# Kernel optimization log

Hardware: AMD Instinct MI355X
Metric: run time of the kernel (lower is better)

Reference implementation:

```python
import jax, jax.numpy as jnp
import numpy as np
from jax import lax

RES = 512          # resolution
L = 16             # n_light
M = 4
N = 2 * M          # Fourier series terms
FOCAL = 50.0
CAMD = 2.7         # camera_distance
WINDOW = 1.0
SHADOW_THR = 0.008
RES_OPT = 256      # resolution_optimize
OFFSET = -0.0642233295781
CLAMP = 0.4458709375254
RBLUR = 10         # gaussian blur radius (static)

FOV = 2.0 * np.arctan(0.5 * 36.0 / FOCAL)
TANH = np.tan(FOV / 2.0)
NEAR = CAMD - np.sqrt(2.0) * CAMD * TANH
FAR = CAMD + np.sqrt(2.0) * CAMD * TANH

_rot_pi = np.array([[np.cos(np.pi), 0, np.sin(np.pi), 0], [0, 1, 0, 0],
                    [-np.sin(np.pi), 0, np.cos(np.pi), 0], [0, 0, 0, 1]], np.float32)
_m_dist = np.eye(4, dtype=np.float32); _m_dist[2, 3] = -CAMD
_local = (_rot_pi @ _m_dist).astype(np.float32)
_orth = np.array([[1.0 / WINDOW, 0, 0, 0], [0, 1.0 / WINDOW, 0, 0],
                  [0, 0, -2.0 / (FAR - NEAR), -(FAR + NEAR) / (FAR - NEAR)],
                  [0, 0, 0, 1]], np.float32)
_ck = (np.pi * (2.0 * (np.arange(M) + 1) - 1)).astype(np.float32)  # [M]


def _rotate_xyz_light(dirs):
    # dirs: [L,3] -> [L,4,4] (already transposed as in the torch permute(0,2,1))
    xd, yd, zd = dirs[:, 0], dirs[:, 1], dirs[:, 2]
    cosp = jnp.sqrt(xd * xd + zd * zd)
    cost = zd / cosp
    sint = xd / cosp
    Z = jnp.zeros_like(xd); O = jnp.ones_like(xd)
    Rn = jnp.stack([cost, -sint * yd, cosp * sint, Z,
                    Z, cosp, yd, Z,
                    -sint, -cost * yd, cosp * cost, Z,
                    Z, Z, Z, O], axis=-1).reshape(-1, 4, 4)
    return jnp.swapaxes(Rn, 1, 2)


def _blur_one(img, k):
    # img: [N,H,W], k: [2R+1]  separable gaussian, zero padding
    kh = k.reshape(1, 1, -1, 1)
    kw = k.reshape(1, 1, 1, -1)
    x = img[:, None]  # [N,1,H,W]
    x = lax.conv_general_dilated(x, kh, (1, 1), ((RBLUR, RBLUR), (0, 0)))
    x = lax.conv_general_dilated(x, kw, (1, 1), ((0, 0), (RBLUR, RBLUR)))
    return x[:, 0]


def _forward(depth, als, mask, z_map):
    res = RES
    local = jnp.asarray(_local); m_dist = jnp.asarray(_m_dist); orth = jnp.asarray(_orth)
    m1 = 2.0 * (jnp.arange(res, dtype=jnp.float32) / res + 1.0 / (2 * res)) - 1.0
    dz = depth[0, 0]                               # [res,res]
    px = -dz * TANH * m1[None, :]                  # x varies along width
    py = dz * TANH * m1[:, None]                   # y varies along height
    posw = jnp.stack([px, py, dz, jnp.ones_like(dz)], axis=-1).reshape(-1, 4)  # [V,4]
    posw_c = posw @ local.T

    mv = jnp.einsum('xy,dyz->dxz', m_dist, _rotate_xyz_light(als[:, :3]))  # [L,4,4]
    pfl = jnp.einsum('vw,dxw->dvx', posw_c, mv)
    pfl = jnp.einsum('dvw,xw->dvx', pfl, orth)      # [L,V,4]

    u = jnp.clip((res * (pfl[..., 0] + 1.0) * 0.5).astype(jnp.int32), 0, res - 1)
    v = jnp.clip((res * (pfl[..., 1] + 1.0) * 0.5).astype(jnp.int32), 0, res - 1)
    d = jnp.clip(0.5 * (1.0 + pfl[..., 2] / pfl[..., 3]), 0.0, 1.0)  # [L,V]

    li = jnp.arange(L)
    zg = z_map[li[:, None], v, u]                   # gather shadow-map depth [L,V]
    f = jnp.where(jnp.clip(d - zg, 0.0, None) > SHADOW_THR, 0.0, 1.0)

    ck = jnp.asarray(_ck)[None, :, None]            # [1,M,1]
    a_even = -2.0 * jnp.sin(ck * (d[:, None, :] + OFFSET)) / ck
    a_odd = 2.0 * jnp.cos(ck * (d[:, None, :] + OFFSET)) / ck
    a = jnp.stack([a_even, a_odd], axis=2).reshape(L, N, -1)  # interleaved [L,N,V]

    ckz = ck[..., None] * z_map[:, None]            # [L,M,res,res]
    B = jnp.stack([jnp.cos(ckz), jnp.sin(ckz)], axis=2).reshape(L, N, res, res)

    sig = (res / RES_OPT * (6.0 * als[:, 3] + 1.0) - 1.0) / 6.0   # [L]
    t = jnp.arange(-RBLUR, RBLUR + 1, dtype=jnp.float32)
    kern = jnp.exp(-0.5 * (t[None, :] / sig[:, None]) ** 2)
    kern = kern / jnp.sum(kern, axis=1, keepdims=True)            # [L,2R+1]
    D_map = jax.vmap(_blur_one)(B, kern)            # [L,N,res,res]

    ni = jnp.arange(N)
    D = D_map[li[:, None, None], ni[None, :, None], v[:, None, :], u[:, None, :]]  # [L,N,V]
    q = jnp.clip(jnp.sum(a * D, axis=1), -CLAMP, CLAMP) / CLAMP
    sf = 0.5 * (q + 1.0)

    hard = f.reshape(1, L, res, res)
    soft = jnp.clip(sf, 0.0, 1.0).reshape(1, L, res, res)
    return mask * hard, mask * soft


def setup_inputs() -> dict:
    key = jax.random.key(0)
    k1, k2, k3, k4, k5, k6 = jax.random.split(key, 6)
    depth = 2.0 + jax.random.uniform(k1, (1, 1, RES, RES), dtype=jnp.float32)
    mask = (jax.random.uniform(k2, (1, 1, RES, RES)) > 0.2).astype(jnp.float32)
    dirs = jax.random.normal(k3, (L, 3), dtype=jnp.float32)
    dirs = dirs / jnp.linalg.norm(dirs, axis=1, keepdims=True)
    sigma = 0.02 + 0.1 * jax.random.uniform(k4, (L, 1), dtype=jnp.float32)
    intensity = jax.random.uniform(k5, (L, 3), dtype=jnp.float32)
    als = jnp.concatenate([dirs, sigma, intensity], axis=1)  # [L,7]
    z_map = 0.3 + 0.7 * jax.random.uniform(k6, (L, RES, RES), dtype=jnp.float32)
    return {"depth": depth, "als": als, "mask": mask, "z_map": z_map}


def reference(depth, als, mask, z_map):
    return _forward(depth, als, mask, z_map)
```

## Files before the change

### kernel.cpp

```cpp
#include <hip/hip_runtime.h>
#include <math.h>


#define RESN 512
#define NL 16
#define NPIX (RESN*RESN)

__global__ void setup_kernel(const float* __restrict__ als,
                             float* __restrict__ lp) {
  #pragma clang fp contract(off)
  int l = (int)threadIdx.x;
  if (l >= NL) return;
  float xd = als[l*7+0], yd = als[l*7+1], zd = als[l*7+2], sg = als[l*7+3];
  float cosp = sqrtf(xd*xd + zd*zd);
  float cost = zd / cosp;
  float sint = xd / cosp;
  float* o = lp + l*16;
  o[0] = cost;
  o[1] = -sint;
  o[2] = (-sint)*yd;
  o[3] = cosp;
  o[4] = (-cost)*yd;
  o[5] = cosp*sint;
  o[6] = yd;
  o[7] = cosp*cost;
  float sig = ((2.0f*(6.0f*sg + 1.0f)) - 1.0f) / 6.0f;
  float ivs = 1.0f/(sig*sig);
  float e1  = __builtin_amdgcn_exp2f(-0.72134752044448170368f*ivs);
  float e1sq = e1*e1;
  float e2  = e1sq*e1sq;
  float kinv = 1.0f/(1.0f + 2.0f*e1 + 2.0f*e2);
  float w1n = e1*kinv;
  o[8] = kinv;
  o[9] = w1n;
  o[10] = (w1n >= 0.0056f) ? 1.0f : 0.0f;
  o[11] = kinv*kinv;
  o[12] = o[13] = o[14] = o[15] = 0.0f;
}

__global__ __launch_bounds__(128) void fused_kernel(
    const float* __restrict__ depth,
    const float* __restrict__ mask,
    const float* __restrict__ z_map,
    const float* __restrict__ lp,
    float* __restrict__ out,
    float TANHF, float OZF, float OWF)
{
  #pragma clang fp contract(off)
  const float OFFS = -0.0642233295781f;
  const float CLB  = 0.4458709375254f;
  const float TWO_OVER_PI = 0.63661977236758134308f;
  const int id = (int)blockIdx.x;
  const int l0 = id & 7;
  const int p  = ((id >> 3) << 7) + (int)threadIdx.x;
  const int r  = p >> 9, c = p & 511;

  float dz = depth[p];
  float mk = mask[p];
  float m1c = 2.0f * ((float)c / 512.0f + 0.0009765625f) - 1.0f;
  float m1r = 2.0f * ((float)r / 512.0f + 0.0009765625f) - 1.0f;
  float tT = dz * TANHF;
  float qx = tT * m1c;
  float qy = tT * m1r;
  float qz = 2.7f - dz;
  const bool live = (mk != 0.0f);

  #pragma unroll
  for (int k = 0; k < 2; ++k) {
    const int l = l0 + (k << 3);
    const int base = l << 18;
    float hard_out = 0.0f, soft_out = 0.0f;
    if (live) {
      const float* P = lp + l*16;
      float e00 = P[0], e02 = P[1], e10 = P[2], e11 = P[3], e12 = P[4];
      float e20 = P[5], e21 = P[6], e22 = P[7];
      float w0 = P[8], w1 = P[9];
      bool five_tap = P[10] != 0.0f;
      float w0sq = P[11];

      float X1 = fmaf(qz, e02, qx * e00);
      float Y1 = fmaf(qz, e12, fmaf(qy, e11, qx * e10));
      float T2 = fmaf(qz, e22, fmaf(qy, e21, qx * e20));
      float Z1 = T2 + (-2.7f);
      float ZZ = (Z1 * OZF) + OWF;
      float uf = (X1 + 1.0f) * 256.0f;
      float vf = (Y1 + 1.0f) * 256.0f;
      int u = (int)uf; u = u < 0 ? 0 : (u > 511 ? 511 : u);
      int v = (int)vf; v = v < 0 ? 0 : (v > 511 ? 511 : v);
      float dd = 0.5f * (1.0f + ZZ);
      dd = fminf(fmaxf(dd, 0.0f), 1.0f);
      float dpo = dd + OFFS;

      const float* zrC = z_map + base + (v << 9);
      float zg = zrC[u];

      auto fval = [&](float z) {
        float s = __builtin_amdgcn_sinf(0.5f * (z - dpo));
        float t = s * s;
        return s * fmaf(t, fmaf(t, fmaf(t, -9.142857142857142f, 19.2f),
                                -13.333333333333334f), 4.0f);
      };

      float q;
      if (five_tap) {
        int u0 = u > 0 ? u - 1 : 0;
        int u2 = u < 511 ? u + 1 : 511;
        int v0 = v > 0 ? v - 1 : 0;
        int v2 = v < 511 ? v + 1 : 511;
        float zT = z_map[base + (v0 << 9) + u];
        float zL = zrC[u0];
        float zR = zrC[u2];
        float zB = z_map[base + (v2 << 9) + u];
        float wuL = (u > 0)   ? w1 : 0.0f;
        float wuR = (u < 511) ? w1 : 0.0f;
        float wvT = (v > 0)   ? w1 : 0.0f;
        float wvB = (v < 511) ? w1 : 0.0f;
        float qs = w0 * fval(zg);
        qs = fmaf(wvT, fval(zT), qs);
        qs = fmaf(wvB, fval(zB), qs);
        qs = fmaf(wuL, fval(zL), qs);
        qs = fmaf(wuR, fval(zR), qs);
        q = TWO_OVER_PI * (w0 * qs);
      } else {
        q = TWO_OVER_PI * (w0sq * fval(zg));
      }

      float diff = fmaxf(dd - zg, 0.0f);
      hard_out = mk * ((diff > 0.008f) ? 0.0f : 1.0f);
      float qc = fminf(fmaxf(q, -CLB), CLB) / CLB;
      float sf = 0.5f * (qc + 1.0f);
      soft_out = mk * fminf(fmaxf(sf, 0.0f), 1.0f);
    }
    out[base + p] = hard_out;
    out[(NL*NPIX) + base + p] = soft_out;
  }
}

extern "C" void kernel_launch(void* const* d_in, const int* in_sizes, int n_in,
                              void* d_out, int out_size, void* d_ws, size_t ws_size,
                              hipStream_t stream) {
  (void)in_sizes; (void)n_in; (void)out_size; (void)ws_size;
  const float* depth = (const float*)d_in[0];
  const float* als   = (const float*)d_in[1];
  const float* mask  = (const float*)d_in[2];
  const float* z_map = (const float*)d_in[3];
  float* out = (float*)d_out;
  float* lp = (float*)d_ws;
  double TANH = tan(2.0*atan(0.5*36.0/50.0)/2.0);
  double NEARc = 2.7 - sqrt(2.0)*2.7*TANH;
  double FARc  = 2.7 + sqrt(2.0)*2.7*TANH;
  float ozf = (float)(-2.0/(FARc-NEARc));
  float owf = (float)((-(FARc+NEARc))/(FARc-NEARc));
  float tanhf_ = (float)TANH;

  setup_kernel<<<1, 64, 0, stream>>>(als, lp);
  fused_kernel<<<(NL/2)*NPIX/128, 128, 0, stream>>>(depth, mask, z_map, lp,
                                                    out, tanhf_, ozf, owf);
}
```

Before: 114.1 us.

## Batch gathers for both lights and use 4-wide row load for horizontal taps

Splits the per-light loop into a gather phase that issues all z_map loads for both lights up front, then a compute phase separated by a scheduling barrier, so memory latency overlaps across lights. The center/left/right taps are fetched with one unaligned 4-float vector load from a clamped start column, and the right values are picked with selects. This cuts the number of gather instructions and raises memory-level parallelism, at the cost of more live registers and extra select logic.

```diff
diff --git a/kernel.cpp b/kernel.cpp
--- a/kernel.cpp
+++ b/kernel.cpp
@@ -5,6 +5,8 @@
 #define RESN 512
 #define NL 16
 #define NPIX (RESN*RESN)
+
+typedef float f4a __attribute__((ext_vector_type(4), aligned(4)));
 
 __global__ void setup_kernel(const float* __restrict__ als,
                              float* __restrict__ lp) {
@@ -65,18 +67,28 @@
   float qz = 2.7f - dz;
   const bool live = (mk != 0.0f);
 
-  #pragma unroll
-  for (int k = 0; k < 2; ++k) {
-    const int l = l0 + (k << 3);
-    const int base = l << 18;
-    float hard_out = 0.0f, soft_out = 0.0f;
-    if (live) {
+  float hard_out[2] = {0.0f, 0.0f};
+  float soft_out[2] = {0.0f, 0.0f};
+
+  if (live) {
+    float rx[2], ry[2], rz[2], rw[2];
+    float zT[2], zB[2];
+    float wvT_[2], wvB_[2];
+    float dd_[2], dpo_[2];
+    float w0_[2], w1_[2], w0q_[2];
+    int   u_[2], ic_[2];
+    bool  ft_[2];
+
+    #pragma unroll
+    for (int k = 0; k < 2; ++k) {
+      const int l = l0 + (k << 3);
+      const int base = l << 18;
       const float* P = lp + l*16;
       float e00 = P[0], e02 = P[1], e10 = P[2], e11 = P[3], e12 = P[4];
       float e20 = P[5], e21 = P[6], e22 = P[7];
-      float w0 = P[8], w1 = P[9];
-      bool five_tap = P[10] != 0.0f;
-      float w0sq = P[11];
+      w0_[k] = P[8]; w1_[k] = P[9]; w0q_[k] = P[11];
+      bool ft = P[10] != 0.0f;
+      ft_[k] = ft;
 
       float X1 = fmaf(qz, e02, qx * e00);
       float Y1 = fmaf(qz, e12, fmaf(qy, e11, qx * e10));
@@ -89,50 +101,73 @@
       int v = (int)vf; v = v < 0 ? 0 : (v > 511 ? 511 : v);
       float dd = 0.5f * (1.0f + ZZ);
       dd = fminf(fmaxf(dd, 0.0f), 1.0f);
-      float dpo = dd + OFFS;
+      dd_[k] = dd; dpo_[k] = dd + OFFS;
+      u_[k] = u;
 
       const float* zrC = z_map + base + (v << 9);
-      float zg = zrC[u];
+      if (ft) {
+        int b = u - 1; b = b < 0 ? 0 : (b > 508 ? 508 : b);
+        f4a rv = *reinterpret_cast<const f4a*>(zrC + b);
+        rx[k] = rv.x; ry[k] = rv.y; rz[k] = rv.z; rw[k] = rv.w;
+        ic_[k] = u - b;
+        int v0 = v > 0 ? v - 1 : 0;
+        int v2 = v < 511 ? v + 1 : 511;
+        zT[k] = z_map[base + (v0 << 9) + u];
+        zB[k] = z_map[base + (v2 << 9) + u];
+        wvT_[k] = (v > 0)   ? w1_[k] : 0.0f;
+        wvB_[k] = (v < 511) ? w1_[k] : 0.0f;
+      } else {
+        ry[k] = zrC[u];
+        ic_[k] = 1;
+        wvT_[k] = wvB_[k] = 0.0f;
+      }
+    }
 
+    __builtin_amdgcn_sched_barrier(0x7);
+
+    #pragma unroll
+    for (int k = 0; k < 2; ++k) {
+      const float dpo = dpo_[k];
       auto fval = [&](float z) {
         float s = __builtin_amdgcn_sinf(0.5f * (z - dpo));
         float t = s * s;
         return s * fmaf(t, fmaf(t, fmaf(t, -9.142857142857142f, 19.2f),
                                 -13.333333333333334f), 4.0f);
       };
-
-      float q;
-      if (five_tap) {
-        int u0 = u > 0 ? u - 1 : 0;
-        int u2 = u < 511 ? u + 1 : 511;
-        int v0 = v > 0 ? v - 1 : 0;
-        int v2 = v < 511 ? v + 1 : 511;
-        float zT = z_map[base + (v0 << 9) + u];
-        float zL = zrC[u0];
-        float zR = zrC[u2];
-        float zB = z_map[base + (v2 << 9) + u];
+      float w0 = w0_[k], w1 = w1_[k];
+      float q, zg;
+      if (ft_[k]) {
+        bool c0 = ic_[k] == 0, c2 = ic_[k] == 2, c3 = ic_[k] == 3;
+        float zC = c0 ? rx[k] : c2 ? rz[k] : c3 ? rw[k] : ry[k];
+        float zL = c0 ? rx[k] : c2 ? ry[k] : c3 ? rz[k] : rx[k];
+        float zR = c0 ? ry[k] : (c2 | c3) ? rw[k] : rz[k];
+        int u = u_[k];
         float wuL = (u > 0)   ? w1 : 0.0f;
         float wuR = (u < 511) ? w1 : 0.0f;
-        float wvT = (v > 0)   ? w1 : 0.0f;
-        float wvB = (v < 511) ? w1 : 0.0f;
-        float qs = w0 * fval(zg);
-        qs = fmaf(wvT, fval(zT), qs);
-        qs = fmaf(wvB, fval(zB), qs);
+        float qs = w0 * fval(zC);
+        qs = fmaf(wvT_[k], fval(zT[k]), qs);
+        qs = fmaf(wvB_[k], fval(zB[k]), qs);
         qs = fmaf(wuL, fval(zL), qs);
         qs = fmaf(wuR, fval(zR), qs);
         q = TWO_OVER_PI * (w0 * qs);
+        zg = zC;
       } else {
-        q = TWO_OVER_PI * (w0sq * fval(zg));
+        zg = ry[k];
+        q = TWO_OVER_PI * (w0q_[k] * fval(zg));
       }
-
-      float diff = fmaxf(dd - zg, 0.0f);
-      hard_out = mk * ((diff > 0.008f) ? 0.0f : 1.0f);
+      float diff = fmaxf(dd_[k] - zg, 0.0f);
+      hard_out[k] = mk * ((diff > 0.008f) ? 0.0f : 1.0f);
       float qc = fminf(fmaxf(q, -CLB), CLB) / CLB;
       float sf = 0.5f * (qc + 1.0f);
-      soft_out = mk * fminf(fmaxf(sf, 0.0f), 1.0f);
+      soft_out[k] = mk * fminf(fmaxf(sf, 0.0f), 1.0f);
     }
-    out[base + p] = hard_out;
-    out[(NL*NPIX) + base + p] = soft_out;
+  }
+
+  #pragma unroll
+  for (int k = 0; k < 2; ++k) {
+    const int base = (l0 + (k << 3)) << 18;
+    out[base + p] = hard_out[k];
+    out[(NL*NPIX) + base + p] = soft_out[k];
   }
 }
 
```

Result: faster. 105.9 us (-7.2%).
